# Kernel tuning notes

Hardware: AMD Instinct MI355X
Metric: run time of the kernel (lower is better)

## Reference

```python
import math
import jax, jax.numpy as jnp
import numpy as np

B, T, C = 4, 2048, 1024
NH = 16
HD = C // NH  # 64

def setup_inputs() -> dict:
    key = jax.random.key(0)
    k1, k2, k3 = jax.random.split(key, 3)
    x = jax.random.normal(k1, (B, T, C), dtype=jnp.float32)
    # init scale ~ 1/sqrt(fan_in) to keep activations sane
    W_attn = jax.random.normal(k2, (C, 3 * C), dtype=jnp.float32) * (1.0 / math.sqrt(C))
    b_attn = jnp.zeros((3 * C,), dtype=jnp.float32)
    W_proj = jax.random.normal(k3, (C, C), dtype=jnp.float32) * (1.0 / math.sqrt(C))
    b_proj = jnp.zeros((C,), dtype=jnp.float32)
    return {"x": x, "W_attn": W_attn, "b_attn": b_attn, "W_proj": W_proj, "b_proj": b_proj}

def reference(x, W_attn, b_attn, W_proj, b_proj):
    b, t, c = x.shape
    qkv = x @ W_attn + b_attn                      # [B,T,3C]
    q, k, v = jnp.split(qkv, 3, axis=-1)           # each [B,T,C]
    # [B,T,C] -> [B,NH,T,HD]
    def heads(z):
        return z.reshape(b, t, NH, HD).transpose(0, 2, 1, 3)
    q, k, v = heads(q), heads(k), heads(v)
    scale = 1.0 / math.sqrt(HD)
    att = jnp.einsum('bhqd,bhkd->bhqk', q, k) * scale   # [B,NH,T,T]
    causal = jnp.tril(jnp.ones((t, t), dtype=bool))      # [T,T]
    att = jnp.where(causal[None, None, :, :], att, -jnp.inf)
    att = jax.nn.softmax(att, axis=-1)
    # dropout p=0.0 -> identity
    y = jnp.einsum('bhqk,bhkd->bhqd', att, v)            # [B,NH,T,HD]
    y = y.transpose(0, 2, 1, 3).reshape(b, t, c)         # [B,T,C]
    return y @ W_proj + b_proj
```

## Files before the change

kernel.cpp:

```cpp
#include <hip/hip_runtime.h>
#include <hip/hip_bf16.h>


typedef __bf16 bf16;
typedef __bf16 bf16x4 __attribute__((ext_vector_type(4)));
typedef __bf16 bf16x8 __attribute__((ext_vector_type(8)));
typedef float  f32x4  __attribute__((ext_vector_type(4)));

#define MFMA16(a, b, c) __builtin_amdgcn_mfma_f32_16x16x32_bf16((a), (b), (c), 0, 0, 0)

#define GLOAD16(g, l)                                                 \
    __builtin_amdgcn_global_load_lds(                                 \
        (const __attribute__((address_space(1))) void*)(g),           \
        (__attribute__((address_space(3))) void*)(l), 16, 0, 0)

static constexpr int Bsz = 4;
static constexpr int T   = 2048;
static constexpr int Cc  = 1024;
static constexpr int NH  = 16;
static constexpr int HD  = 64;
static constexpr int C3  = 3 * Cc;

__global__ void cvt_f32_bf16(const float* __restrict__ in, bf16* __restrict__ out) {
    size_t i = ((size_t)blockIdx.x * blockDim.x + threadIdx.x) * 8;
    f32x4 a0 = *(const f32x4*)(in + i);
    f32x4 a1 = *(const f32x4*)(in + i + 4);
    bf16x8 v;
#pragma unroll
    for (int e = 0; e < 4; ++e) { v[e] = (bf16)a0[e]; v[e + 4] = (bf16)a1[e]; }
    *(bf16x8*)(out + i) = v;
}

__global__ void transpose_f32_bf16(const float* __restrict__ in, bf16* __restrict__ out,
                                   int R, int Ccols) {
    __shared__ float tile[32][33];
    int bx = blockIdx.x * 32;
    int by = blockIdx.y * 32;
    int tx = threadIdx.x, ty = threadIdx.y;
#pragma unroll
    for (int i = 0; i < 32; i += 8)
        tile[ty + i][tx] = in[(size_t)(by + ty + i) * Ccols + bx + tx];
    __syncthreads();
#pragma unroll
    for (int i = 0; i < 32; i += 8)
        out[(size_t)(bx + ty + i) * R + by + tx] = (bf16)tile[tx][ty + i];
}

__global__ __launch_bounds__(256)
void gemm_qkv(const bf16* __restrict__ A, const bf16* __restrict__ Bt,
              const float* __restrict__ bias,
              bf16* __restrict__ qo, bf16* __restrict__ ko, bf16* __restrict__ vt,
              int M, int N, int K) {
    constexpr int BM = 128, BN = 128, BK = 64;
    __shared__ bf16 As[BM * BK];
    __shared__ bf16 Bs[BN * BK];

    const int tid  = threadIdx.x;
    const int wave = tid >> 6, lane = tid & 63;
    const int quad = lane >> 4, l16 = lane & 15;
    const int wm = wave & 1, wn = wave >> 1;
    const int m0 = blockIdx.x * BM, n0 = blockIdx.y * BN;

    f32x4 acc[4][4] = {};

    const int lrow = lane >> 3;
    const int lcol = (lane & 7) * 8;
    const bf16* Ab = A  + (size_t)(m0 + wave * 8 + lrow) * K + lcol;
    const bf16* Bb = Bt + (size_t)(n0 + wave * 8 + lrow) * K + lcol;
    bf16* Asw = As + wave * 512;
    bf16* Bsw = Bs + wave * 512;

    for (int k0 = 0; k0 < K; k0 += BK) {
#pragma unroll
        for (int r = 0; r < 4; ++r)
            GLOAD16(Ab + (size_t)r * 32 * K + k0, Asw + r * 2048);
#pragma unroll
        for (int r = 0; r < 4; ++r)
            GLOAD16(Bb + (size_t)r * 32 * K + k0, Bsw + r * 2048);
        __syncthreads();

#pragma unroll
        for (int ks = 0; ks < 2; ++ks) {
            bf16x8 af[4], bfr[4];
#pragma unroll
            for (int i = 0; i < 4; ++i)
                af[i] = *(const bf16x8*)(&As[(wm * 64 + i * 16 + l16) * BK + ks * 32 + quad * 8]);
#pragma unroll
            for (int j = 0; j < 4; ++j)
                bfr[j] = *(const bf16x8*)(&Bs[(wn * 64 + j * 16 + l16) * BK + ks * 32 + quad * 8]);
#pragma unroll
            for (int i = 0; i < 4; ++i)
#pragma unroll
                for (int j = 0; j < 4; ++j)
                    acc[i][j] = MFMA16(af[i], bfr[j], acc[i][j]);
        }
        __syncthreads();
    }

    const int which = n0 >> 10;
    const int nc0 = n0 & 1023;
    if (which < 2) {
        bf16* dst = which ? ko : qo;
#pragma unroll
        for (int j = 0; j < 4; ++j) {
            int colg = n0 + wn * 64 + j * 16 + l16;
            int coll = nc0 + wn * 64 + j * 16 + l16;
            float bv = bias[colg];
#pragma unroll
            for (int i = 0; i < 4; ++i) {
                int rowb = m0 + wm * 64 + i * 16 + quad * 4;
#pragma unroll
                for (int r = 0; r < 4; ++r)
                    dst[(size_t)(rowb + r) * Cc + coll] = (bf16)(acc[i][j][r] + bv);
            }
        }
    } else {
#pragma unroll
        for (int j = 0; j < 4; ++j) {
            int colg = n0 + wn * 64 + j * 16 + l16;
            int coll = nc0 + wn * 64 + j * 16 + l16;
            int h = coll >> 6, d = coll & 63;
            float bv = bias[colg];
            bf16* vhead_d = vt + ((size_t)h * HD + d) * T;
#pragma unroll
            for (int i = 0; i < 4; ++i) {
                int rowb = m0 + wm * 64 + i * 16 + quad * 4;
                int b = rowb >> 11;
                int t = rowb & 2047;
                bf16x4 pk;
#pragma unroll
                for (int r = 0; r < 4; ++r) pk[r] = (bf16)(acc[i][j][r] + bv);
                *(bf16x4*)(vhead_d + (size_t)b * NH * HD * T + t) = pk;
            }
        }
    }
}

__global__ __launch_bounds__(256)
void gemm_bt(const bf16* __restrict__ A, const bf16* __restrict__ Bt,
             const float* __restrict__ bias, float* __restrict__ C,
             int M, int N, int K) {
    constexpr int BM = 128, BN = 128, BK = 64;
    __shared__ bf16 As[BM * BK];
    __shared__ bf16 Bs[BN * BK];

    const int tid  = threadIdx.x;
    const int wave = tid >> 6, lane = tid & 63;
    const int quad = lane >> 4, l16 = lane & 15;
    const int wm = wave & 1, wn = wave >> 1;
    const int m0 = blockIdx.x * BM, n0 = blockIdx.y * BN;

    f32x4 acc[4][4] = {};

    const int lrow = lane >> 3;
    const int lcol = (lane & 7) * 8;
    const bf16* Ab = A  + (size_t)(m0 + wave * 8 + lrow) * K + lcol;
    const bf16* Bb = Bt + (size_t)(n0 + wave * 8 + lrow) * K + lcol;
    bf16* Asw = As + wave * 512;
    bf16* Bsw = Bs + wave * 512;

    for (int k0 = 0; k0 < K; k0 += BK) {
#pragma unroll
        for (int r = 0; r < 4; ++r)
            GLOAD16(Ab + (size_t)r * 32 * K + k0, Asw + r * 2048);
#pragma unroll
        for (int r = 0; r < 4; ++r)
            GLOAD16(Bb + (size_t)r * 32 * K + k0, Bsw + r * 2048);
        __syncthreads();

#pragma unroll
        for (int ks = 0; ks < 2; ++ks) {
            bf16x8 af[4], bfr[4];
#pragma unroll
            for (int i = 0; i < 4; ++i)
                af[i] = *(const bf16x8*)(&As[(wm * 64 + i * 16 + l16) * BK + ks * 32 + quad * 8]);
#pragma unroll
            for (int j = 0; j < 4; ++j)
                bfr[j] = *(const bf16x8*)(&Bs[(wn * 64 + j * 16 + l16) * BK + ks * 32 + quad * 8]);
#pragma unroll
            for (int i = 0; i < 4; ++i)
#pragma unroll
                for (int j = 0; j < 4; ++j)
                    acc[i][j] = MFMA16(af[i], bfr[j], acc[i][j]);
        }
        __syncthreads();
    }

#pragma unroll
    for (int j = 0; j < 4; ++j) {
        int col = n0 + wn * 64 + j * 16 + l16;
        float bv = bias[col];
#pragma unroll
        for (int i = 0; i < 4; ++i) {
            int rowb = m0 + wm * 64 + i * 16 + quad * 4;
#pragma unroll
            for (int r = 0; r < 4; ++r)
                C[(size_t)(rowb + r) * N + col] = acc[i][j][r] + bv;
        }
    }
}

__global__ __launch_bounds__(256)
void attn_fused(const bf16* __restrict__ qb, const bf16* __restrict__ kb,
                const bf16* __restrict__ vtb, bf16* __restrict__ y) {
    constexpr int LKD = 72, LVT = 72, LPS = 72;
    constexpr int QT = T / 128;
    __shared__ bf16 Ks[64 * LKD];
    __shared__ bf16 Vt[64 * LVT];
    __shared__ bf16 Ps[4][32 * LPS];

    const int tid  = threadIdx.x;
    const int wave = tid >> 6, lane = tid & 63;
    const int quad = lane >> 4, l16 = lane & 15;
    const int pr = blockIdx.x;
    const int b = blockIdx.y >> 4, h = blockIdx.y & 15;

    const bf16* qbase  = qb + (size_t)b * T * Cc + h * HD;
    const bf16* kbase  = kb + (size_t)b * T * Cc + h * HD;
    const bf16* vthead = vtb + (size_t)(b * NH + h) * HD * T;
    bf16* yrow = y + (size_t)b * T * Cc + h * HD;

    const int srow = tid >> 2;
    const int sch  = tid & 3;

#pragma unroll 1
    for (int seg = 0; seg < 2; ++seg) {
        const int qt = (seg == 0) ? (QT - 1 - pr) : pr;
        const int q0 = qt * 128;

        bf16x8 qf[2][2];
#pragma unroll
        for (int qn = 0; qn < 2; ++qn) {
            int qrow = q0 + wave * 32 + qn * 16 + l16;
#pragma unroll
            for (int ks = 0; ks < 2; ++ks) {
                bf16x8 v = *(const bf16x8*)(qbase + (size_t)qrow * Cc + ks * 32 + quad * 8);
#pragma unroll
                for (int e = 0; e < 8; ++e) v[e] = (bf16)((float)v[e] * 0.18033688f);
                qf[qn][ks] = v;
            }
        }

        f32x4 o[2][4] = {};
        float lsum[2] = {0.f, 0.f};

        const int w0 = q0 + wave * 32;
        const int nt = q0 / 64 + 2;

        bf16x8 kp[2], vp[2];
#pragma unroll
        for (int c2 = 0; c2 < 2; ++c2) {
            int ch = sch + c2 * 4;
            kp[c2] = *(const bf16x8*)(kbase + (size_t)srow * Cc + ch * 8);
            vp[c2] = *(const bf16x8*)(vthead + (size_t)srow * T + ch * 8);
        }

        for (int it = 0; it < nt; ++it) {
            const int kt = it * 64;
#pragma unroll
            for (int c2 = 0; c2 < 2; ++c2) {
                int ch = sch + c2 * 4;
                *(bf16x8*)(&Ks[srow * LKD + ch * 8]) = kp[c2];
                *(bf16x8*)(&Vt[srow * LVT + ch * 8]) = vp[c2];
            }
            __syncthreads();

            if (it + 1 < nt) {
                int ktn = kt + 64;
#pragma unroll
                for (int c2 = 0; c2 < 2; ++c2) {
                    int ch = sch + c2 * 4;
                    kp[c2] = *(const bf16x8*)(kbase + (size_t)(ktn + srow) * Cc + ch * 8);
                    vp[c2] = *(const bf16x8*)(vthead + (size_t)srow * T + ktn + ch * 8);
                }
            }

            if (kt <= w0 + 31) {
                f32x4 st[4][2] = {};
#pragma unroll
                for (int km = 0; km < 4; ++km) {
                    bf16x8 kf0 = *(const bf16x8*)(&Ks[(km * 16 + l16) * LKD + quad * 8]);
                    bf16x8 kf1 = *(const bf16x8*)(&Ks[(km * 16 + l16) * LKD + 32 + quad * 8]);
#pragma unroll
                    for (int qn = 0; qn < 2; ++qn) {
                        st[km][qn] = MFMA16(kf0, qf[qn][0], st[km][qn]);
                        st[km][qn] = MFMA16(kf1, qf[qn][1], st[km][qn]);
                    }
                }

                const bool needmask = (kt + 63 > w0);
                float rs[2] = {0.f, 0.f};
#pragma unroll
                for (int km = 0; km < 4; ++km)
#pragma unroll
                    for (int qn = 0; qn < 2; ++qn) {
                        int qrel = w0 + qn * 16 + l16 - kt;
#pragma unroll
                        for (int r = 0; r < 4; ++r) {
                            float v = st[km][qn][r];
                            if (needmask) {
                                int key = km * 16 + quad * 4 + r;
                                v = (key <= qrel) ? v : -INFINITY;
                            }
                            float p = __builtin_exp2f(fminf(v, 115.0f));
                            st[km][qn][r] = p;
                            rs[qn] += p;
                        }
                    }
#pragma unroll
                for (int qn = 0; qn < 2; ++qn) {
                    rs[qn] += __shfl_xor(rs[qn], 16, 64);
                    rs[qn] += __shfl_xor(rs[qn], 32, 64);
                    lsum[qn] += rs[qn];
                }

                bf16* pw = &Ps[wave][0];
#pragma unroll
                for (int qn = 0; qn < 2; ++qn)
#pragma unroll
                    for (int km = 0; km < 4; ++km) {
                        bf16x4 pk;
#pragma unroll
                        for (int r = 0; r < 4; ++r) pk[r] = (bf16)st[km][qn][r];
                        *(bf16x4*)(&pw[(qn * 16 + l16) * LPS + km * 16 + quad * 4]) = pk;
                    }
                bf16x8 pf[2][2];
#pragma unroll
                for (int qn = 0; qn < 2; ++qn)
#pragma unroll
                    for (int ks = 0; ks < 2; ++ks)
                        pf[qn][ks] = *(const bf16x8*)(&pw[(qn * 16 + l16) * LPS + ks * 32 + quad * 8]);

#pragma unroll
                for (int dd = 0; dd < 4; ++dd)
#pragma unroll
                    for (int ks = 0; ks < 2; ++ks) {
                        bf16x8 vf = *(const bf16x8*)(&Vt[(dd * 16 + l16) * LVT + ks * 32 + quad * 8]);
                        o[0][dd] = MFMA16(pf[0][ks], vf, o[0][dd]);
                        o[1][dd] = MFMA16(pf[1][ks], vf, o[1][dd]);
                    }
            }
            __syncthreads();
        }

#pragma unroll
        for (int qn = 0; qn < 2; ++qn)
#pragma unroll
            for (int r = 0; r < 4; ++r) {
                float den = __shfl(lsum[qn], (lane & 48) | (quad * 4 + r), 64);
                float inv = 1.0f / den;
                int t = w0 + qn * 16 + quad * 4 + r;
#pragma unroll
                for (int dd = 0; dd < 4; ++dd)
                    yrow[(size_t)t * Cc + dd * 16 + l16] = (bf16)(o[qn][dd][r] * inv);
            }
    }
}

extern "C" void kernel_launch(void* const* d_in, const int* in_sizes, int n_in,
                              void* d_out, int out_size, void* d_ws, size_t ws_size,
                              hipStream_t stream) {
    const float* x      = (const float*)d_in[0];
    const float* W_attn = (const float*)d_in[1];
    const float* b_attn = (const float*)d_in[2];
    const float* W_proj = (const float*)d_in[3];
    const float* b_proj = (const float*)d_in[4];
    float* out = (float*)d_out;

    const int M = Bsz * T;
    const size_t R = (size_t)M * Cc;

    bf16* qb  = (bf16*)d_ws;
    bf16* kb  = qb + R;
    bf16* vtb = kb + R;
    bf16* xb  = vtb + R;
    bf16* yb  = xb;
    bf16* WtA = (bf16*)d_out;
    bf16* WtP = qb;

    dim3 tpb(32, 8);

    cvt_f32_bf16<<<(int)(R / (256 * 8)), 256, 0, stream>>>(x, xb);
    transpose_f32_bf16<<<dim3(C3 / 32, Cc / 32), tpb, 0, stream>>>(W_attn, WtA, Cc, C3);
    gemm_qkv<<<dim3(M / 128, C3 / 128), 256, 0, stream>>>(xb, WtA, b_attn, qb, kb, vtb, M, C3, Cc);
    attn_fused<<<dim3(T / 256, Bsz * NH), 256, 0, stream>>>(qb, kb, vtb, yb);
    transpose_f32_bf16<<<dim3(Cc / 32, Cc / 32), tpb, 0, stream>>>(W_proj, WtP, Cc, Cc);
    gemm_bt<<<dim3(M / 128, Cc / 128), 256, 0, stream>>>(yb, WtP, b_proj, out, M, Cc, Cc);
}
```

Before: 301.7 us.

## Double-buffer LDS tiles in GEMMs and attention, remap attention grid

Both GEMM kernels now keep two LDS stages and issue the async global-to-LDS loads for the next K tile before computing on the current one. This removes one barrier per iteration and overlaps memory traffic with MFMA work. The attention kernel double-buffers its K/V tiles, raises wave priority during compute, drops the exp2 clamp, and flattens the grid so consecutive blocks cover different heads for the same query-pair index. The trade-off is doubled LDS use, which may lower occupancy. Removing the clamp could also risk overflow if scores exceed the exp2 range.

```diff
diff --git a/kernel.cpp b/kernel.cpp
--- a/kernel.cpp
+++ b/kernel.cpp
@@ -52,8 +52,8 @@
               bf16* __restrict__ qo, bf16* __restrict__ ko, bf16* __restrict__ vt,
               int M, int N, int K) {
     constexpr int BM = 128, BN = 128, BK = 64;
-    __shared__ bf16 As[BM * BK];
-    __shared__ bf16 Bs[BN * BK];
+    __shared__ bf16 As[2][BM * BK];
+    __shared__ bf16 Bs[2][BN * BK];
 
     const int tid  = threadIdx.x;
     const int wave = tid >> 6, lane = tid & 63;
@@ -67,34 +67,42 @@
     const int lcol = (lane & 7) * 8;
     const bf16* Ab = A  + (size_t)(m0 + wave * 8 + lrow) * K + lcol;
     const bf16* Bb = Bt + (size_t)(n0 + wave * 8 + lrow) * K + lcol;
-    bf16* Asw = As + wave * 512;
-    bf16* Bsw = Bs + wave * 512;
-
+    const int wofs = wave * 512;
+
+#pragma unroll
+    for (int r = 0; r < 4; ++r) {
+        GLOAD16(Ab + (size_t)r * 32 * K, As[0] + wofs + r * 2048);
+        GLOAD16(Bb + (size_t)r * 32 * K, Bs[0] + wofs + r * 2048);
+    }
+
+    int cur = 0;
     for (int k0 = 0; k0 < K; k0 += BK) {
-#pragma unroll
-        for (int r = 0; r < 4; ++r)
-            GLOAD16(Ab + (size_t)r * 32 * K + k0, Asw + r * 2048);
-#pragma unroll
-        for (int r = 0; r < 4; ++r)
-            GLOAD16(Bb + (size_t)r * 32 * K + k0, Bsw + r * 2048);
         __syncthreads();
-
+        if (k0 + BK < K) {
+#pragma unroll
+            for (int r = 0; r < 4; ++r) {
+                GLOAD16(Ab + (size_t)r * 32 * K + k0 + BK, As[cur ^ 1] + wofs + r * 2048);
+                GLOAD16(Bb + (size_t)r * 32 * K + k0 + BK, Bs[cur ^ 1] + wofs + r * 2048);
+            }
+        }
+        const bf16* Asc = As[cur];
+        const bf16* Bsc = Bs[cur];
 #pragma unroll
         for (int ks = 0; ks < 2; ++ks) {
             bf16x8 af[4], bfr[4];
 #pragma unroll
             for (int i = 0; i < 4; ++i)
-                af[i] = *(const bf16x8*)(&As[(wm * 64 + i * 16 + l16) * BK + ks * 32 + quad * 8]);
+                af[i] = *(const bf16x8*)(&Asc[(wm * 64 + i * 16 + l16) * BK + ks * 32 + quad * 8]);
 #pragma unroll
             for (int j = 0; j < 4; ++j)
-                bfr[j] = *(const bf16x8*)(&Bs[(wn * 64 + j * 16 + l16) * BK + ks * 32 + quad * 8]);
+                bfr[j] = *(const bf16x8*)(&Bsc[(wn * 64 + j * 16 + l16) * BK + ks * 32 + quad * 8]);
 #pragma unroll
             for (int i = 0; i < 4; ++i)
 #pragma unroll
                 for (int j = 0; j < 4; ++j)
                     acc[i][j] = MFMA16(af[i], bfr[j], acc[i][j]);
         }
-        __syncthreads();
+        cur ^= 1;
     }
 
     const int which = n0 >> 10;
@@ -141,8 +149,8 @@
              const float* __restrict__ bias, float* __restrict__ C,
              int M, int N, int K) {
     constexpr int BM = 128, BN = 128, BK = 64;
-    __shared__ bf16 As[BM * BK];
-    __shared__ bf16 Bs[BN * BK];
+    __shared__ bf16 As[2][BM * BK];
+    __shared__ bf16 Bs[2][BN * BK];
 
     const int tid  = threadIdx.x;
     const int wave = tid >> 6, lane = tid & 63;
@@ -156,34 +164,42 @@
     const int lcol = (lane & 7) * 8;
     const bf16* Ab = A  + (size_t)(m0 + wave * 8 + lrow) * K + lcol;
     const bf16* Bb = Bt + (size_t)(n0 + wave * 8 + lrow) * K + lcol;
-    bf16* Asw = As + wave * 512;
-    bf16* Bsw = Bs + wave * 512;
-
+    const int wofs = wave * 512;
+
+#pragma unroll
+    for (int r = 0; r < 4; ++r) {
+        GLOAD16(Ab + (size_t)r * 32 * K, As[0] + wofs + r * 2048);
+        GLOAD16(Bb + (size_t)r * 32 * K, Bs[0] + wofs + r * 2048);
+    }
+
+    int cur = 0;
     for (int k0 = 0; k0 < K; k0 += BK) {
-#pragma unroll
-        for (int r = 0; r < 4; ++r)
-            GLOAD16(Ab + (size_t)r * 32 * K + k0, Asw + r * 2048);
-#pragma unroll
-        for (int r = 0; r < 4; ++r)
-            GLOAD16(Bb + (size_t)r * 32 * K + k0, Bsw + r * 2048);
         __syncthreads();
-
+        if (k0 + BK < K) {
+#pragma unroll
+            for (int r = 0; r < 4; ++r) {
+                GLOAD16(Ab + (size_t)r * 32 * K + k0 + BK, As[cur ^ 1] + wofs + r * 2048);
+                GLOAD16(Bb + (size_t)r * 32 * K + k0 + BK, Bs[cur ^ 1] + wofs + r * 2048);
+            }
+        }
+        const bf16* Asc = As[cur];
+        const bf16* Bsc = Bs[cur];
 #pragma unroll
         for (int ks = 0; ks < 2; ++ks) {
             bf16x8 af[4], bfr[4];
 #pragma unroll
             for (int i = 0; i < 4; ++i)
-                af[i] = *(const bf16x8*)(&As[(wm * 64 + i * 16 + l16) * BK + ks * 32 + quad * 8]);
+                af[i] = *(const bf16x8*)(&Asc[(wm * 64 + i * 16 + l16) * BK + ks * 32 + quad * 8]);
 #pragma unroll
             for (int j = 0; j < 4; ++j)
-                bfr[j] = *(const bf16x8*)(&Bs[(wn * 64 + j * 16 + l16) * BK + ks * 32 + quad * 8]);
+                bfr[j] = *(const bf16x8*)(&Bsc[(wn * 64 + j * 16 + l16) * BK + ks * 32 + quad * 8]);
 #pragma unroll
             for (int i = 0; i < 4; ++i)
 #pragma unroll
                 for (int j = 0; j < 4; ++j)
                     acc[i][j] = MFMA16(af[i], bfr[j], acc[i][j]);
         }
-        __syncthreads();
+        cur ^= 1;
     }
 
 #pragma unroll
@@ -205,15 +221,17 @@
                 const bf16* __restrict__ vtb, bf16* __restrict__ y) {
     constexpr int LKD = 72, LVT = 72, LPS = 72;
     constexpr int QT = T / 128;
-    __shared__ bf16 Ks[64 * LKD];
-    __shared__ bf16 Vt[64 * LVT];
+    __shared__ bf16 Ks[2][64 * LKD];
+    __shared__ bf16 Vt[2][64 * LVT];
     __shared__ bf16 Ps[4][32 * LPS];
 
     const int tid  = threadIdx.x;
     const int wave = tid >> 6, lane = tid & 63;
     const int quad = lane >> 4, l16 = lane & 15;
-    const int pr = blockIdx.x;
-    const int b = blockIdx.y >> 4, h = blockIdx.y & 15;
+    const int bid = blockIdx.x;
+    const int pr = bid >> 6;
+    const int hb = bid & 63;
+    const int b = hb >> 4, h = hb & 15;
 
     const bf16* qbase  = qb + (size_t)b * T * Cc + h * HD;
     const bf16* kbase  = kb + (size_t)b * T * Cc + h * HD;
@@ -254,18 +272,21 @@
             kp[c2] = *(const bf16x8*)(kbase + (size_t)srow * Cc + ch * 8);
             vp[c2] = *(const bf16x8*)(vthead + (size_t)srow * T + ch * 8);
         }
-
+        __syncthreads();
+#pragma unroll
+        for (int c2 = 0; c2 < 2; ++c2) {
+            int ch = sch + c2 * 4;
+            *(bf16x8*)(&Ks[0][srow * LKD + ch * 8]) = kp[c2];
+            *(bf16x8*)(&Vt[0][srow * LVT + ch * 8]) = vp[c2];
+        }
+
+        int cur = 0;
         for (int it = 0; it < nt; ++it) {
             const int kt = it * 64;
-#pragma unroll
-            for (int c2 = 0; c2 < 2; ++c2) {
-                int ch = sch + c2 * 4;
-                *(bf16x8*)(&Ks[srow * LKD + ch * 8]) = kp[c2];
-                *(bf16x8*)(&Vt[srow * LVT + ch * 8]) = vp[c2];
-            }
             __syncthreads();
 
-            if (it + 1 < nt) {
+            const bool more = (it + 1 < nt);
+            if (more) {
                 int ktn = kt + 64;
 #pragma unroll
                 for (int c2 = 0; c2 < 2; ++c2) {
@@ -275,12 +296,15 @@
                 }
             }
 
+            const bf16* ksc = Ks[cur];
+            const bf16* vtc = Vt[cur];
             if (kt <= w0 + 31) {
+                __builtin_amdgcn_s_setprio(1);
                 f32x4 st[4][2] = {};
 #pragma unroll
                 for (int km = 0; km < 4; ++km) {
-                    bf16x8 kf0 = *(const bf16x8*)(&Ks[(km * 16 + l16) * LKD + quad * 8]);
-                    bf16x8 kf1 = *(const bf16x8*)(&Ks[(km * 16 + l16) * LKD + 32 + quad * 8]);
+                    bf16x8 kf0 = *(const bf16x8*)(&ksc[(km * 16 + l16) * LKD + quad * 8]);
+                    bf16x8 kf1 = *(const bf16x8*)(&ksc[(km * 16 + l16) * LKD + 32 + quad * 8]);
 #pragma unroll
                     for (int qn = 0; qn < 2; ++qn) {
                         st[km][qn] = MFMA16(kf0, qf[qn][0], st[km][qn]);
@@ -302,7 +326,7 @@
                                 int key = km * 16 + quad * 4 + r;
                                 v = (key <= qrel) ? v : -INFINITY;
                             }
-                            float p = __builtin_exp2f(fminf(v, 115.0f));
+                            float p = __builtin_exp2f(v);
                             st[km][qn][r] = p;
                             rs[qn] += p;
                         }
@@ -335,12 +359,22 @@
                 for (int dd = 0; dd < 4; ++dd)
 #pragma unroll
                     for (int ks = 0; ks < 2; ++ks) {
-                        bf16x8 vf = *(const bf16x8*)(&Vt[(dd * 16 + l16) * LVT + ks * 32 + quad * 8]);
+                        bf16x8 vf = *(const bf16x8*)(&vtc[(dd * 16 + l16) * LVT + ks * 32 + quad * 8]);
                         o[0][dd] = MFMA16(pf[0][ks], vf, o[0][dd]);
                         o[1][dd] = MFMA16(pf[1][ks], vf, o[1][dd]);
                     }
-            }
-            __syncthreads();
+                __builtin_amdgcn_s_setprio(0);
+            }
+
+            if (more) {
+#pragma unroll
+                for (int c2 = 0; c2 < 2; ++c2) {
+                    int ch = sch + c2 * 4;
+                    *(bf16x8*)(&Ks[cur ^ 1][srow * LKD + ch * 8]) = kp[c2];
+                    *(bf16x8*)(&Vt[cur ^ 1][srow * LVT + ch * 8]) = vp[c2];
+                }
+            }
+            cur ^= 1;
         }
 
 #pragma unroll
@@ -383,7 +417,7 @@
     cvt_f32_bf16<<<(int)(R / (256 * 8)), 256, 0, stream>>>(x, xb);
     transpose_f32_bf16<<<dim3(C3 / 32, Cc / 32), tpb, 0, stream>>>(W_attn, WtA, Cc, C3);
     gemm_qkv<<<dim3(M / 128, C3 / 128), 256, 0, stream>>>(xb, WtA, b_attn, qb, kb, vtb, M, C3, Cc);
-    attn_fused<<<dim3(T / 256, Bsz * NH), 256, 0, stream>>>(qb, kb, vtb, yb);
+    attn_fused<<<512, 256, 0, stream>>>(qb, kb, vtb, yb);
     transpose_f32_bf16<<<dim3(Cc / 32, Cc / 32), tpb, 0, stream>>>(W_proj, WtP, Cc, Cc);
     gemm_bt<<<dim3(M / 128, Cc / 128), 256, 0, stream>>>(yb, WtP, b_proj, out, M, Cc, Cc);
 }
```

Measured after the change: 286.4 us. 5.0% less time.
